# Kernel optimization log

Hardware: AMD Instinct MI355X
Metric: run time of the kernel (lower is better)

## Reference

```python
import jax, jax.numpy as jnp
import numpy as np

D_MODEL = 1024
NUM_HEADS = 16
NUM_GROUPS = 4
HEAD_DIM = D_MODEL // NUM_HEADS
ROPE_BASE = 10000.0


def _rope_tables(seq_len, head_dim, dtype=jnp.float32):
    inv_freq = 1.0 / (ROPE_BASE ** (jnp.arange(0, head_dim, 2, dtype=jnp.float32) / head_dim))
    freqs = jnp.arange(seq_len, dtype=jnp.float32)[:, None] * inv_freq[None, :]  # [S, hd/2]
    emb = jnp.concatenate([freqs, freqs], axis=-1)  # [S, hd]
    return jnp.cos(emb).astype(dtype), jnp.sin(emb).astype(dtype)


def _rotate_half(t):
    half = t.shape[-1] // 2
    return jnp.concatenate([-t[..., half:], t[..., :half]], axis=-1)


def _apply_rope(t, cos, sin):
    # t: [B,S,H,hd]; cos/sin: [S,hd] broadcast over batch and heads
    c = cos[None, :, None, :]
    s = sin[None, :, None, :]
    return t * c + _rotate_half(t) * s


def setup_inputs() -> dict:
    key = jax.random.key(0)
    ks = jax.random.split(key, 5)
    B, S, D = 2, 2048, D_MODEL
    scale = 1.0 / np.sqrt(D)
    return {
        "x": jax.random.normal(ks[0], (B, S, D), dtype=jnp.float32),
        "Wq": jax.random.normal(ks[1], (D, D), dtype=jnp.float32) * scale,
        "Wk": jax.random.normal(ks[2], (D, D), dtype=jnp.float32) * scale,
        "Wv": jax.random.normal(ks[3], (D, D), dtype=jnp.float32) * scale,
        "Wo": jax.random.normal(ks[4], (D, D), dtype=jnp.float32) * scale,
    }


def reference(x, Wq, Wk, Wv, Wo):
    B, S, D = x.shape
    H, G, hd = NUM_HEADS, NUM_GROUPS, HEAD_DIM
    hpg = H // G  # heads per group

    q = (x @ Wq.T).reshape(B, S, H, hd)
    k = (x @ Wk.T).reshape(B, S, H, hd)
    v = (x @ Wv.T).reshape(B, S, H, hd)

    cos, sin = _rope_tables(S, hd, x.dtype)
    q = _apply_rope(q, cos, sin)
    k = _apply_rope(k, cos, sin)

    # query head reordering: [B,S,G,hpg,hd] -> transpose(2,3) -> [B,S,H,hd]
    q = q.reshape(B, S, G, hpg, hd).swapaxes(2, 3).reshape(B, S, H, hd)
    # GQA group-mean of K/V, then repeat back to H heads
    k = k.reshape(B, S, G, hpg, hd).mean(axis=3)  # [B,S,G,hd]
    v = v.reshape(B, S, G, hpg, hd).mean(axis=3)
    k = jnp.repeat(k, hpg, axis=2)  # [B,S,H,hd]
    v = jnp.repeat(v, hpg, axis=2)

    q = q.transpose(0, 2, 1, 3)  # [B,H,S,hd]
    k = k.transpose(0, 2, 1, 3)
    v = v.transpose(0, 2, 1, 3)

    scores = jnp.einsum('bhqd,bhkd->bhqk', q, k) / np.sqrt(hd)  # [B,H,S,S]
    probs = jax.nn.softmax(scores, axis=-1)
    attn = jnp.einsum('bhqk,bhkd->bhqd', probs, v)

    attn = attn.transpose(0, 2, 1, 3).reshape(B, S, D)
    return attn @ Wo.T
```

## Files before the change

### kernel.cpp

```cpp
#include <hip/hip_runtime.h>
#include <hip/hip_bf16.h>
#include <math.h>

#define B_ 2
#define S_ 2048
#define D_ 1024
#define H_ 16
#define G_ 4
#define HD_ 64

typedef float f32x4  __attribute__((ext_vector_type(4)));
typedef float f32x16 __attribute__((ext_vector_type(16)));
typedef short s16x8  __attribute__((ext_vector_type(8)));
typedef unsigned short u16x4 __attribute__((ext_vector_type(4)));
typedef unsigned int   u32x4 __attribute__((ext_vector_type(4)));

__device__ __forceinline__ unsigned short f2b(float f) {
    __hip_bfloat16 h = __float2bfloat16(f);
    return __builtin_bit_cast(unsigned short, h);
}
__device__ __forceinline__ unsigned cvtpk(float lo, float hi) {
    unsigned r;
    asm("v_cvt_pk_bf16_f32 %0, %1, %2" : "=v"(r) : "v"(lo), "v"(hi));
    return r;
}
__device__ __forceinline__ void plswap(unsigned &a, unsigned &b) {
    asm("v_permlane32_swap_b32 %0, %1" : "+v"(a), "+v"(b));
}

#define MFMA16(a, b, c) __builtin_amdgcn_mfma_f32_16x16x32_bf16(a, b, c, 0, 0, 0)
#define MFMA32(a, b, c) __builtin_amdgcn_mfma_f32_32x32x16_bf16(a, b, c, 0, 0, 0)

#define GLOAD16(gp, lp) __builtin_amdgcn_global_load_lds(                      \
    (const __attribute__((address_space(1))) void*)(gp),                      \
    (__attribute__((address_space(3))) void*)(lp), 16, 0, 0)

__global__ __launch_bounds__(256)
void prep_all(const float* __restrict__ x,  const float* __restrict__ Wq,
              const float* __restrict__ Wk, const float* __restrict__ Wv,
              const float* __restrict__ Wo,
              unsigned short* __restrict__ xb, unsigned short* __restrict__ wb,
              unsigned short* __restrict__ wob,
              float* __restrict__ cost, float* __restrict__ sint)
{
    const int NQ_WB = (1536*1024)/4;
    const int NQ_WO = (1024*1024)/4;
    const int NQ_X  = (B_*S_*D_)/4;
    int q = blockIdx.x*256 + threadIdx.x;
    if (q < NQ_WB) {
        const int idx = q*4, row = idx >> 10, c = idx & 1023;
        u16x4 o;
        if (row < 1024) {
            f32x4 v = *(const f32x4*)&Wq[(size_t)row*1024 + c];
            #pragma unroll
            for (int j = 0; j < 4; ++j) o[j] = f2b(v[j]);
        } else {
            const int rd = row - 1024, kv = rd >> 8, gd = rd & 255;
            const int g = gd >> 6, d = gd & 63;
            const float* W = kv ? Wv : Wk;
            f32x4 sum = {0.f, 0.f, 0.f, 0.f};
            #pragma unroll
            for (int p = 0; p < 4; ++p)
                sum += *(const f32x4*)&W[(size_t)((g*4 + p)*64 + d)*1024 + c];
            #pragma unroll
            for (int j = 0; j < 4; ++j) o[j] = f2b(sum[j]*0.25f);
        }
        *(u16x4*)&wb[idx] = o;
        return;
    }
    q -= NQ_WB;
    if (q < NQ_WO) {
        const int idx = q*4;
        f32x4 v = *(const f32x4*)&Wo[idx];
        u16x4 o;
        #pragma unroll
        for (int j = 0; j < 4; ++j) o[j] = f2b(v[j]);
        *(u16x4*)&wob[idx] = o;
        return;
    }
    q -= NQ_WO;
    if (q < NQ_X) {
        const int idx = q*4;
        f32x4 v = *(const f32x4*)&x[idx];
        u16x4 o;
        #pragma unroll
        for (int j = 0; j < 4; ++j) o[j] = f2b(v[j]);
        *(u16x4*)&xb[idx] = o;
        return;
    }
    q -= NQ_X;
    if (q < (S_*32)/4) {
        const int idx = q*4, s = idx >> 5, f0 = idx & 31;
        #pragma unroll
        for (int j = 0; j < 4; ++j) {
            const float f = (float)(f0 + j);
            const float fr = (float)s * powf(10000.0f, -f*(1.0f/32.0f));
            cost[idx + j] = cosf(fr);
            sint[idx + j] = sinf(fr);
        }
    }
}

template<int MODE>
__global__ __launch_bounds__(256)
void gemm_mfma(const unsigned short* __restrict__ Am,
               const unsigned short* __restrict__ Bm,
               unsigned short* __restrict__ qr,
               unsigned short* __restrict__ kr,
               unsigned short* __restrict__ vt,
               float* __restrict__ outf,
               const float* __restrict__ cost,
               const float* __restrict__ sint,
               int nbx)
{
    __shared__ unsigned short As[2][64*64];
    __shared__ unsigned short Bs[2][128*64];

    const int nwg = gridDim.x;
    const int cpx = nwg >> 3;
    const int bid = blockIdx.x;
    const int swz = (bid & 7)*cpx + (bid >> 3);
    const int bx = swz % nbx, by = swz / nbx;

    const int t  = threadIdx.x;
    const int w  = t >> 6, l = t & 63;
    const int lg = l >> 4, lr = l & 15;
    const int wr = w >> 1, wc = w & 1;

    const unsigned short* gA = Am + (size_t)by*64*D_;
    const unsigned short* gB = Bm + (size_t)bx*128*D_;

    const int srow = l >> 3;
    const int schk = (l & 7) ^ srow;

#define STAGE(buf, k0)                                                         \
    _Pragma("unroll")                                                          \
    for (int i_ = 0; i_ < 2; ++i_) {                                           \
        const int rowA_ = 16*w + 8*i_ + srow;                                  \
        GLOAD16(gA + (size_t)rowA_*D_ + (k0) + 8*schk, &As[buf][(16*w + 8*i_)*64]); \
    }                                                                          \
    _Pragma("unroll")                                                          \
    for (int i_ = 0; i_ < 4; ++i_) {                                           \
        const int rowB_ = 32*w + 8*i_ + srow;                                  \
        GLOAD16(gB + (size_t)rowB_*D_ + (k0) + 8*schk, &Bs[buf][(32*w + 8*i_)*64]); \
    }

    f32x4 acc[2][4] = {};

    STAGE(0, 0);
    #pragma unroll 1
    for (int kt = 0; kt < 16; ++kt) {
        const int cur = kt & 1;
        if (kt < 15) {
            STAGE(cur ^ 1, 64*(kt + 1));
            asm volatile("s_waitcnt vmcnt(6)" ::: "memory");
        } else {
            asm volatile("s_waitcnt vmcnt(0)" ::: "memory");
        }
        __builtin_amdgcn_s_barrier();

        #pragma unroll
        for (int kk = 0; kk < 2; ++kk) {
            s16x8 af[2], bfr[4];
            #pragma unroll
            for (int m = 0; m < 2; ++m) {
                const int row = 32*wr + 16*m + lr;
                af[m] = *(const s16x8*)&As[cur][row*64 + 8*((lg + 4*kk) ^ (row & 7))];
            }
            #pragma unroll
            for (int n = 0; n < 4; ++n) {
                const int col = 64*wc + 16*n + lr;
                bfr[n] = *(const s16x8*)&Bs[cur][col*64 + 8*((lg + 4*kk) ^ (col & 7))];
            }
            #pragma unroll
            for (int m = 0; m < 2; ++m)
                #pragma unroll
                for (int n = 0; n < 4; ++n)
                    acc[m][n] = MFMA16(af[m], bfr[n], acc[m][n]);
        }
        asm volatile("s_waitcnt lgkmcnt(0)" ::: "memory");
        __builtin_amdgcn_s_barrier();
    }
#undef STAGE

    if (MODE == 1) {
        #pragma unroll
        for (int m = 0; m < 2; ++m)
            #pragma unroll
            for (int r = 0; r < 4; ++r) {
                const int row = by*64 + 32*wr + 16*m + 4*lg + r;
                #pragma unroll
                for (int n = 0; n < 4; ++n)
                    outf[(size_t)row*D_ + bx*128 + 64*wc + 16*n + lr] = acc[m][n][r];
            }
        return;
    }

    if (bx < 10) {
        const float CQ = 0.18033688011112044f;
        #pragma unroll
        for (int m = 0; m < 2; ++m) {
            #pragma unroll
            for (int r = 0; r < 4; ++r) {
                const int row = by*64 + 32*wr + 16*m + 4*lg + r;
                const int b = row >> 11, s = row & (S_ - 1);
                const float c_lo = cost[s*32 + lr],      s_lo = sint[s*32 + lr];
                const float c_hi = cost[s*32 + 16 + lr], s_hi = sint[s*32 + 16 + lr];
                unsigned short vals[4];
                #pragma unroll
                for (int n = 0; n < 4; ++n) {
                    const float cc = (n & 1) ? c_hi : c_lo;
                    const float sn = (n & 1) ? s_hi : s_lo;
                    const float self = acc[m][n][r], part = acc[m][n ^ 2][r];
                    float rv = (n < 2) ? fmaf(self, cc, -part*sn)
                                       : fmaf(self, cc,  part*sn);
                    if (bx < 8) rv *= CQ;
                    vals[n] = f2b(rv);
                }
                size_t base;
                unsigned short* dst;
                if (bx < 8) {
                    const int hh = 2*bx + wc;
                    const int hp = (hh & 3)*4 + (hh >> 2);
                    base = (((size_t)b*H_ + hp)*S_ + s)*HD_;
                    dst = qr;
                } else {
                    const int g = (bx - 8)*2 + wc;
                    base = (((size_t)b*G_ + g)*S_ + s)*HD_;
                    dst = kr;
                }
                #pragma unroll
                for (int n = 0; n < 4; ++n) dst[base + 16*n + lr] = vals[n];
            }
        }
    } else {
        const int g = (bx - 10)*2 + wc;
        #pragma unroll
        for (int m = 0; m < 2; ++m) {
            const int row0 = by*64 + 32*wr + 16*m + 4*lg;
            const int b = row0 >> 11, s0 = row0 & (S_ - 1);
            #pragma unroll
            for (int n = 0; n < 4; ++n) {
                const int dd = 16*n + lr;
                u16x4 v;
                #pragma unroll
                for (int r = 0; r < 4; ++r) v[r] = f2b(acc[m][n][r]);
                *(u16x4*)&vt[(((size_t)b*G_ + g)*HD_ + dd)*S_ + s0] = v;
            }
        }
    }
}

__device__ __forceinline__ void stage64(const unsigned short* Kp, const unsigned short* Vp,
                                        unsigned short* ks, unsigned short* vs,
                                        int key0, int w, int l)
{
    const int srow = l >> 3;
    const int schk = (l & 7) ^ srow;
    #pragma unroll
    for (int i = 0; i < 2; ++i) {
        const int row = 16*w + 8*i + srow;
        GLOAD16(Kp + ((size_t)(key0 + row))*HD_ + 8*schk, ks + (16*w + 8*i)*64);
        GLOAD16(Vp + (size_t)row*S_ + key0 + 8*schk,      vs + (16*w + 8*i)*64);
    }
}

__global__ __launch_bounds__(256, 2)
void flash_attn_mfma(const unsigned short* __restrict__ qr,
                     const unsigned short* __restrict__ kr,
                     const unsigned short* __restrict__ vt,
                     unsigned short* __restrict__ attnb)
{
    __shared__ unsigned short KsA[2][64*64];
    __shared__ unsigned short VsA[2][64*64];
    __shared__ unsigned short KsB[2][64*64];
    __shared__ unsigned short VsB[2][64*64];

    const int bid = blockIdx.x;
    const int cpx = gridDim.x >> 3;
    const int swz = (bid & 7)*cpx + (bid >> 3);
    const int qt  = swz & 15;
    const int h   = (swz >> 4) & 15;
    const int b   = swz >> 8;
    const int g   = h >> 2;
    const int t   = threadIdx.x;
    const int w   = t >> 6;
    const int l   = t & 63;
    const int hi  = l >> 5;
    const int li  = l & 31;

    const unsigned short* Qp  = qr + (((size_t)b*H_ + h)*S_ + (size_t)qt*128 + w*32)*HD_;
    const unsigned short* KpA = kr + ((size_t)b*G_ + g)*(size_t)S_*HD_;
    const unsigned short* VpA = vt + ((size_t)b*G_ + g)*(size_t)HD_*S_;
    const unsigned short* KpB = KpA + (size_t)1024*HD_;
    const unsigned short* VpB = VpA + 1024;

    s16x8 qf[4];
    #pragma unroll
    for (int kk = 0; kk < 4; ++kk)
        qf[kk] = *(const s16x8*)(Qp + (size_t)li*HD_ + 16*kk + 8*hi);

    s16x8 ones;
    #pragma unroll
    for (int e = 0; e < 8; ++e) ones[e] = (short)0x3F80;

    f32x16 oA[2], oB[2], olA, olB;
    #pragma unroll
    for (int e = 0; e < 16; ++e) {
        oA[0][e] = 0.f; oA[1][e] = 0.f; olA[e] = 0.f;
        oB[0][e] = 0.f; oB[1][e] = 0.f; olB[e] = 0.f;
    }

    const int NT = 1024/64;
    stage64(KpA, VpA, KsA[0], VsA[0], 0, w, l);
    stage64(KpB, VpB, KsB[0], VsB[0], 0, w, l);

    #pragma unroll 1
    for (int kt = 0; kt < NT; ++kt) {
        const int cur = kt & 1;
        if (kt + 1 < NT) {
            stage64(KpA, VpA, KsA[cur^1], VsA[cur^1], 64*(kt + 1), w, l);
            stage64(KpB, VpB, KsB[cur^1], VsB[cur^1], 64*(kt + 1), w, l);
            asm volatile("s_waitcnt vmcnt(8)" ::: "memory");
        } else {
            asm volatile("s_waitcnt vmcnt(0)" ::: "memory");
        }
        __builtin_amdgcn_s_barrier();

        f32x16 scA[2], scB[2];
        #pragma unroll
        for (int q4 = 0; q4 < 2; ++q4)
            #pragma unroll
            for (int e = 0; e < 16; ++e) { scA[q4][e] = 0.f; scB[q4][e] = 0.f; }

        __builtin_amdgcn_s_setprio(1);
        #pragma unroll
        for (int kk = 0; kk < 4; ++kk) {
            const int chk = 8*((hi + 2*kk) ^ (li & 7));
            #pragma unroll
            for (int q4 = 0; q4 < 2; ++q4) {
                s16x8 kfA = *(const s16x8*)&KsA[cur][(32*q4 + li)*64 + chk];
                scA[q4] = MFMA32(kfA, qf[kk], scA[q4]);
            }
        }
        #pragma unroll
        for (int kk = 0; kk < 4; ++kk) {
            const int chk = 8*((hi + 2*kk) ^ (li & 7));
            #pragma unroll
            for (int q4 = 0; q4 < 2; ++q4) {
                s16x8 kfB = *(const s16x8*)&KsB[cur][(32*q4 + li)*64 + chk];
                scB[q4] = MFMA32(kfB, qf[kk], scB[q4]);
            }
        }
        __builtin_amdgcn_s_setprio(0);

        #pragma unroll
        for (int q4 = 0; q4 < 2; ++q4)
            #pragma unroll
            for (int e = 0; e < 16; ++e)
                scA[q4][e] = __builtin_amdgcn_exp2f(scA[q4][e]);

        __builtin_amdgcn_s_setprio(1);
        #pragma unroll
        for (int q4 = 0; q4 < 2; ++q4) {
            #pragma unroll
            for (int s2 = 0; s2 < 2; ++s2) {
                unsigned a0 = cvtpk(scA[q4][8*s2+0], scA[q4][8*s2+1]);
                unsigned a1 = cvtpk(scA[q4][8*s2+2], scA[q4][8*s2+3]);
                unsigned a2 = cvtpk(scA[q4][8*s2+4], scA[q4][8*s2+5]);
                unsigned a3 = cvtpk(scA[q4][8*s2+6], scA[q4][8*s2+7]);
                plswap(a0, a2); plswap(a1, a3);
                u32x4 aw = {a0, a1, a2, a3};
                s16x8 paf = __builtin_bit_cast(s16x8, aw);
                const int ks = 2*q4 + s2;
                #pragma unroll
                for (int dt = 0; dt < 2; ++dt) {
                    const int d = li + 32*dt;
                    s16x8 vf = *(const s16x8*)&VsA[cur][d*64 + 8*((hi + 2*ks) ^ (li & 7))];
                    oA[dt] = MFMA32(paf, vf, oA[dt]);
                }
                olA = MFMA32(paf, ones, olA);
            }
        }
        __builtin_amdgcn_s_setprio(0);

        #pragma unroll
        for (int q4 = 0; q4 < 2; ++q4)
            #pragma unroll
            for (int e = 0; e < 16; ++e)
                scB[q4][e] = __builtin_amdgcn_exp2f(scB[q4][e]);

        __builtin_amdgcn_s_setprio(1);
        #pragma unroll
        for (int q4 = 0; q4 < 2; ++q4) {
            #pragma unroll
            for (int s2 = 0; s2 < 2; ++s2) {
                unsigned b0 = cvtpk(scB[q4][8*s2+0], scB[q4][8*s2+1]);
                unsigned b1 = cvtpk(scB[q4][8*s2+2], scB[q4][8*s2+3]);
                unsigned b2 = cvtpk(scB[q4][8*s2+4], scB[q4][8*s2+5]);
                unsigned b3 = cvtpk(scB[q4][8*s2+6], scB[q4][8*s2+7]);
                plswap(b0, b2); plswap(b1, b3);
                u32x4 bw = {b0, b1, b2, b3};
                s16x8 pbf = __builtin_bit_cast(s16x8, bw);
                const int ks = 2*q4 + s2;
                #pragma unroll
                for (int dt = 0; dt < 2; ++dt) {
                    const int d = li + 32*dt;
                    s16x8 vf = *(const s16x8*)&VsB[cur][d*64 + 8*((hi + 2*ks) ^ (li & 7))];
                    oB[dt] = MFMA32(pbf, vf, oB[dt]);
                }
                olB = MFMA32(pbf, ones, olB);
            }
        }
        __builtin_amdgcn_s_setprio(0);

        asm volatile("s_waitcnt lgkmcnt(0)" ::: "memory");
        __builtin_amdgcn_s_barrier();
    }

    #pragma unroll
    for (int r = 0; r < 16; ++r) {
        const int qq = (r & 3) + 8*(r >> 2) + 4*hi;
        const int s  = qt*128 + w*32 + qq;
        const float inv = 1.0f / (olA[r] + olB[r]);
        #pragma unroll
        for (int dt = 0; dt < 2; ++dt)
            attnb[((size_t)b*S_ + s)*D_ + h*HD_ + li + 32*dt] =
                f2b((oA[dt][r] + oB[dt][r]) * inv);
    }
}

extern "C" void kernel_launch(void* const* d_in, const int* in_sizes, int n_in,
                              void* d_out, int out_size, void* d_ws, size_t ws_size,
                              hipStream_t stream)
{
    const float* x  = (const float*)d_in[0];
    const float* Wq = (const float*)d_in[1];
    const float* Wk = (const float*)d_in[2];
    const float* Wv = (const float*)d_in[3];
    const float* Wo = (const float*)d_in[4];
    float* out = (float*)d_out;

    char* p = (char*)d_ws;
    unsigned short* xb    = (unsigned short*)p; p += (size_t)B_*S_*D_*2;
    unsigned short* wb    = (unsigned short*)p; p += (size_t)1536*1024*2;
    unsigned short* wob   = (unsigned short*)p; p += (size_t)1024*1024*2;
    unsigned short* qr    = (unsigned short*)p; p += (size_t)B_*H_*S_*HD_*2;
    unsigned short* kr    = (unsigned short*)p; p += (size_t)B_*G_*S_*HD_*2;
    unsigned short* vt    = (unsigned short*)p; p += (size_t)B_*G_*HD_*S_*2;
    unsigned short* attnb = (unsigned short*)p; p += (size_t)B_*S_*D_*2;
    float* cost = (float*)p; p += (size_t)S_*32*4;
    float* sint = (float*)p;

    prep_all<<<6720, 256, 0, stream>>>(x, Wq, Wk, Wv, Wo, xb, wb, wob, cost, sint);
    gemm_mfma<0><<<64*12, 256, 0, stream>>>(xb, wb, qr, kr, vt, nullptr, cost, sint, 12);
    flash_attn_mfma<<<B_*H_*(S_/128), 256, 0, stream>>>(qr, kr, vt, attnb);
    gemm_mfma<1><<<64*8, 256, 0, stream>>>(attnb, wob, nullptr, nullptr, nullptr, out, cost, sint, 8);
}
```

Measured before the change: 92.56 us.

## Single barrier per tile, pre-summed row-sum MFMA, interleaved QK loads

Restructures the attention inner loop so there is one barrier per key tile, placed before the next tile's prefetch, instead of waiting on partial loads and a second trailing barrier. The probability row sums are reduced in registers first and fed to a single ones-MFMA per half, instead of one per sub-block, which cuts MFMA count for the denominator. The QK loop seeds its accumulators with a zero vector and interleaves the A and B key loads. The single barrier waits on all outstanding loads, which may expose more global-load latency because the prefetch is now issued after the wait. Pre-summing in fp32 then rounding to bf16 also slightly changes the normaliser's rounding.

```diff
diff --git a/kernel.cpp b/kernel.cpp
--- a/kernel.cpp
+++ b/kernel.cpp
@@ -304,6 +304,10 @@
     #pragma unroll
     for (int e = 0; e < 8; ++e) ones[e] = (short)0x3F80;
 
+    f32x16 zf;
+    #pragma unroll
+    for (int e = 0; e < 16; ++e) zf[e] = 0.f;
+
     f32x16 oA[2], oB[2], olA, olB;
     #pragma unroll
     for (int e = 0; e < 16; ++e) {
@@ -315,108 +319,91 @@
     stage64(KpA, VpA, KsA[0], VsA[0], 0, w, l);
     stage64(KpB, VpB, KsB[0], VsB[0], 0, w, l);
 
+#define SOFTPV(sc, Vsb, oacc, olacc)                                           \
+    {                                                                          \
+        _Pragma("unroll")                                                      \
+        for (int q4 = 0; q4 < 2; ++q4)                                         \
+            _Pragma("unroll")                                                  \
+            for (int e = 0; e < 16; ++e)                                       \
+                sc[q4][e] = __builtin_amdgcn_exp2f(sc[q4][e]);                 \
+        float ss[8];                                                           \
+        _Pragma("unroll")                                                      \
+        for (int j = 0; j < 8; ++j)                                            \
+            ss[j] = (sc[0][j] + sc[0][8+j]) + (sc[1][j] + sc[1][8+j]);         \
+        __builtin_amdgcn_s_setprio(1);                                         \
+        _Pragma("unroll")                                                      \
+        for (int q4 = 0; q4 < 2; ++q4) {                                       \
+            _Pragma("unroll")                                                  \
+            for (int s2 = 0; s2 < 2; ++s2) {                                   \
+                unsigned a0 = cvtpk(sc[q4][8*s2+0], sc[q4][8*s2+1]);           \
+                unsigned a1 = cvtpk(sc[q4][8*s2+2], sc[q4][8*s2+3]);           \
+                unsigned a2 = cvtpk(sc[q4][8*s2+4], sc[q4][8*s2+5]);           \
+                unsigned a3 = cvtpk(sc[q4][8*s2+6], sc[q4][8*s2+7]);           \
+                plswap(a0, a2); plswap(a1, a3);                                \
+                u32x4 aw = {a0, a1, a2, a3};                                   \
+                s16x8 paf = __builtin_bit_cast(s16x8, aw);                     \
+                const int ks_ = 2*q4 + s2;                                     \
+                _Pragma("unroll")                                              \
+                for (int dt = 0; dt < 2; ++dt) {                               \
+                    const int d_ = li + 32*dt;                                 \
+                    s16x8 vf = *(const s16x8*)&Vsb[d_*64 + 8*((hi + 2*ks_) ^ (li & 7))]; \
+                    oacc[dt] = MFMA32(paf, vf, oacc[dt]);                      \
+                }                                                              \
+            }                                                                  \
+        }                                                                      \
+        {                                                                      \
+            unsigned a0 = cvtpk(ss[0], ss[1]);                                 \
+            unsigned a1 = cvtpk(ss[2], ss[3]);                                 \
+            unsigned a2 = cvtpk(ss[4], ss[5]);                                 \
+            unsigned a3 = cvtpk(ss[6], ss[7]);                                 \
+            plswap(a0, a2); plswap(a1, a3);                                    \
+            u32x4 aw = {a0, a1, a2, a3};                                       \
+            olacc = MFMA32(__builtin_bit_cast(s16x8, aw), ones, olacc);        \
+        }                                                                      \
+        __builtin_amdgcn_s_setprio(0);                                         \
+    }
+
     #pragma unroll 1
     for (int kt = 0; kt < NT; ++kt) {
         const int cur = kt & 1;
+        asm volatile("s_waitcnt vmcnt(0)" ::: "memory");
+        __builtin_amdgcn_s_barrier();
         if (kt + 1 < NT) {
             stage64(KpA, VpA, KsA[cur^1], VsA[cur^1], 64*(kt + 1), w, l);
             stage64(KpB, VpB, KsB[cur^1], VsB[cur^1], 64*(kt + 1), w, l);
-            asm volatile("s_waitcnt vmcnt(8)" ::: "memory");
-        } else {
-            asm volatile("s_waitcnt vmcnt(0)" ::: "memory");
-        }
-        __builtin_amdgcn_s_barrier();
+        }
 
         f32x16 scA[2], scB[2];
-        #pragma unroll
-        for (int q4 = 0; q4 < 2; ++q4)
-            #pragma unroll
-            for (int e = 0; e < 16; ++e) { scA[q4][e] = 0.f; scB[q4][e] = 0.f; }
-
         __builtin_amdgcn_s_setprio(1);
-        #pragma unroll
-        for (int kk = 0; kk < 4; ++kk) {
+        {
+            const int chk = 8*(hi ^ (li & 7));
+            s16x8 ka0 = *(const s16x8*)&KsA[cur][(     li)*64 + chk];
+            s16x8 ka1 = *(const s16x8*)&KsA[cur][(32 + li)*64 + chk];
+            s16x8 kb0 = *(const s16x8*)&KsB[cur][(     li)*64 + chk];
+            s16x8 kb1 = *(const s16x8*)&KsB[cur][(32 + li)*64 + chk];
+            scA[0] = MFMA32(ka0, qf[0], zf);
+            scA[1] = MFMA32(ka1, qf[0], zf);
+            scB[0] = MFMA32(kb0, qf[0], zf);
+            scB[1] = MFMA32(kb1, qf[0], zf);
+        }
+        #pragma unroll
+        for (int kk = 1; kk < 4; ++kk) {
             const int chk = 8*((hi + 2*kk) ^ (li & 7));
-            #pragma unroll
-            for (int q4 = 0; q4 < 2; ++q4) {
-                s16x8 kfA = *(const s16x8*)&KsA[cur][(32*q4 + li)*64 + chk];
-                scA[q4] = MFMA32(kfA, qf[kk], scA[q4]);
-            }
-        }
-        #pragma unroll
-        for (int kk = 0; kk < 4; ++kk) {
-            const int chk = 8*((hi + 2*kk) ^ (li & 7));
-            #pragma unroll
-            for (int q4 = 0; q4 < 2; ++q4) {
-                s16x8 kfB = *(const s16x8*)&KsB[cur][(32*q4 + li)*64 + chk];
-                scB[q4] = MFMA32(kfB, qf[kk], scB[q4]);
-            }
+            s16x8 ka0 = *(const s16x8*)&KsA[cur][(     li)*64 + chk];
+            s16x8 ka1 = *(const s16x8*)&KsA[cur][(32 + li)*64 + chk];
+            s16x8 kb0 = *(const s16x8*)&KsB[cur][(     li)*64 + chk];
+            s16x8 kb1 = *(const s16x8*)&KsB[cur][(32 + li)*64 + chk];
+            scA[0] = MFMA32(ka0, qf[kk], scA[0]);
+            scA[1] = MFMA32(ka1, qf[kk], scA[1]);
+            scB[0] = MFMA32(kb0, qf[kk], scB[0]);
+            scB[1] = MFMA32(kb1, qf[kk], scB[1]);
         }
         __builtin_amdgcn_s_setprio(0);
 
-        #pragma unroll
-        for (int q4 = 0; q4 < 2; ++q4)
-            #pragma unroll
-            for (int e = 0; e < 16; ++e)
-                scA[q4][e] = __builtin_amdgcn_exp2f(scA[q4][e]);
-
-        __builtin_amdgcn_s_setprio(1);
-        #pragma unroll
-        for (int q4 = 0; q4 < 2; ++q4) {
-            #pragma unroll
-            for (int s2 = 0; s2 < 2; ++s2) {
-                unsigned a0 = cvtpk(scA[q4][8*s2+0], scA[q4][8*s2+1]);
-                unsigned a1 = cvtpk(scA[q4][8*s2+2], scA[q4][8*s2+3]);
-                unsigned a2 = cvtpk(scA[q4][8*s2+4], scA[q4][8*s2+5]);
-                unsigned a3 = cvtpk(scA[q4][8*s2+6], scA[q4][8*s2+7]);
-                plswap(a0, a2); plswap(a1, a3);
-                u32x4 aw = {a0, a1, a2, a3};
-                s16x8 paf = __builtin_bit_cast(s16x8, aw);
-                const int ks = 2*q4 + s2;
-                #pragma unroll
-                for (int dt = 0; dt < 2; ++dt) {
-                    const int d = li + 32*dt;
-                    s16x8 vf = *(const s16x8*)&VsA[cur][d*64 + 8*((hi + 2*ks) ^ (li & 7))];
-                    oA[dt] = MFMA32(paf, vf, oA[dt]);
-                }
-                olA = MFMA32(paf, ones, olA);
-            }
-        }
-        __builtin_amdgcn_s_setprio(0);
-
-        #pragma unroll
-        for (int q4 = 0; q4 < 2; ++q4)
-            #pragma unroll
-            for (int e = 0; e < 16; ++e)
-                scB[q4][e] = __builtin_amdgcn_exp2f(scB[q4][e]);
-
-        __builtin_amdgcn_s_setprio(1);
-        #pragma unroll
-        for (int q4 = 0; q4 < 2; ++q4) {
-            #pragma unroll
-            for (int s2 = 0; s2 < 2; ++s2) {
-                unsigned b0 = cvtpk(scB[q4][8*s2+0], scB[q4][8*s2+1]);
-                unsigned b1 = cvtpk(scB[q4][8*s2+2], scB[q4][8*s2+3]);
-                unsigned b2 = cvtpk(scB[q4][8*s2+4], scB[q4][8*s2+5]);
-                unsigned b3 = cvtpk(scB[q4][8*s2+6], scB[q4][8*s2+7]);
-                plswap(b0, b2); plswap(b1, b3);
-                u32x4 bw = {b0, b1, b2, b3};
-                s16x8 pbf = __builtin_bit_cast(s16x8, bw);
-                const int ks = 2*q4 + s2;
-                #pragma unroll
-                for (int dt = 0; dt < 2; ++dt) {
-                    const int d = li + 32*dt;
-                    s16x8 vf = *(const s16x8*)&VsB[cur][d*64 + 8*((hi + 2*ks) ^ (li & 7))];
-                    oB[dt] = MFMA32(pbf, vf, oB[dt]);
-                }
-                olB = MFMA32(pbf, ones, olB);
-            }
-        }
-        __builtin_amdgcn_s_setprio(0);
-
-        asm volatile("s_waitcnt lgkmcnt(0)" ::: "memory");
-        __builtin_amdgcn_s_barrier();
-    }
+        SOFTPV(scA, VsA[cur], oA, olA);
+        SOFTPV(scB, VsB[cur], oB, olB);
+    }
+#undef SOFTPV
 
     #pragma unroll
     for (int r = 0; r < 16; ++r) {
```

Result: no change. 91.76 us (-0.9%).
